# Kernel tuning notes

Measured on AMD Instinct MI355X. Metric: run time of the kernel, lower is better.

The kernel has to match this reference:

```python
import jax, jax.numpy as jnp
import numpy as np

L = 2        # rnn_layers
H = 512      # hidden size
T_MAX = 20   # text_max_len
V = 10000    # NUM_WORDS
B = 32       # batch
S = 49       # spatial positions (7x7)


def setup_inputs() -> dict:
    key = jax.random.key(0)
    ks = jax.random.split(key, 12)
    w = lambda k, shape: jax.random.normal(k, shape, dtype=jnp.float32) * 0.02
    return {
        "img_channels": jax.random.normal(ks[0], (B, 512, 7, 7), dtype=jnp.float32),
        "pooled": jax.random.normal(ks[1], (B, H), dtype=jnp.float32),
        "embed_table": w(ks[2], (V, H)),
        "Wq": w(ks[3], (H, H)), "bq": jnp.zeros((H,), jnp.float32),
        "Wk": w(ks[4], (S, S)), "bk": jnp.zeros((S,), jnp.float32),
        "Wv": w(ks[5], (S, S)), "bv": jnp.zeros((S,), jnp.float32),
        "Wih": w(ks[6], (L, 4 * H, H)), "Whh": w(ks[7], (L, 4 * H, H)),
        "bih": jnp.zeros((L, 4 * H), jnp.float32), "bhh": jnp.zeros((L, 4 * H), jnp.float32),
        "projW": w(ks[8], (V, H)), "projb": jnp.zeros((V,), jnp.float32),
        "hattW": w(ks[9], (H, 2 * H)), "hattb": jnp.zeros((H,), jnp.float32),
        "sos_idx": 1,
    }


def _lstm_cell(x, h, c, wih, whh, bi, bh):
    # PyTorch gate order: i, f, g, o
    g = x @ wih.T + bi + h @ whh.T + bh
    i, f, gg, o = jnp.split(g, 4, axis=-1)
    c2 = jax.nn.sigmoid(f) * c + jax.nn.sigmoid(i) * jnp.tanh(gg)
    return jax.nn.sigmoid(o) * jnp.tanh(c2), c2


def reference(img_channels, pooled, embed_table, Wq, bq, Wk, bk, Wv, bv,
              Wih, Whh, bih, bhh, projW, projb, hattW, hattb, sos_idx):
    Bsz = img_channels.shape[0]
    chan = img_channels.reshape(Bsz, 512, -1)           # [B,512,49]
    # keys/values are step-invariant: precompute once
    keys = jnp.tanh(chan @ Wk.T + bk)                    # [B,512,49]
    values = jnp.tanh(chan @ Wv.T + bv)                  # [B,512,49]

    emb0 = jnp.broadcast_to(embed_table[sos_idx], (Bsz, H))   # <SOS> embedding
    h0 = jnp.broadcast_to(pooled[None], (L, Bsz, H))
    c0 = h0

    def step(carry, _):
        emb, h, c = carry
        x = emb
        hs, cs = [], []
        for l in range(L):  # small fixed layer count
            hl, cl = _lstm_cell(x, h[l], c[l], Wih[l], Whh[l], bih[l], bhh[l])
            hs.append(hl); cs.append(cl)
            x = hl
        out = x                                          # [B,H] top-layer output
        h = jnp.stack(hs); c = jnp.stack(cs)
        # greedy next-token embedding (no teacher forcing)
        logits = out @ projW.T + projb                   # [B,V]
        emb_next = embed_table[jnp.argmax(logits, axis=-1)]
        # cross-attention gated hidden update (all layers at once)
        q = jnp.tanh(h @ Wq.T + bq)                      # [L,B,H]
        scores = jnp.einsum('lbd,bds->lbs', q, keys) / 7.0
        w = jax.nn.softmax(scores, axis=-1)              # [L,B,49]
        attn = jnp.einsum('lbs,bds->lbd', w, values)     # [L,B,H]
        h = jnp.tanh(jnp.concatenate([attn, h], axis=-1) @ hattW.T + hattb)
        return (emb_next, h, c), out

    _, outs = jax.lax.scan(step, (emb0, h0, c0), None, length=T_MAX - 1)
    pred = jnp.concatenate([emb0[None], outs], axis=0)   # [T,B,H]
    res = jnp.einsum('tbd,vd->bvt', pred, projW) + projb[None, :, None]
    return res                                           # [B,V,T]
```

## Files before the change

kernel.cpp:

```cpp
#include <hip/hip_runtime.h>

namespace {

constexpr int B = 32, H = 512, L = 2, T = 20, V = 10000, S = 49;

__device__ __forceinline__ float sigf(float x) { return 1.0f / (1.0f + expf(-x)); }
__device__ __forceinline__ float dot4(float4 a, float4 b) {
  return a.x*b.x + a.y*b.y + a.z*b.z + a.w*b.w;
}

__global__ __launch_bounds__(256) void setup_kernel(
    const float* __restrict__ chan,
    const float* __restrict__ Wk, const float* __restrict__ bk,
    const float* __restrict__ Wv, const float* __restrict__ bv,
    float* __restrict__ keysT, float* __restrict__ valuesT,
    const float* __restrict__ pooled, const float* __restrict__ embed,
    const int* __restrict__ sos,
    float* __restrict__ emb, float* __restrict__ h, float* __restrict__ c,
    const float* __restrict__ projW, const float* __restrict__ projb,
    float* __restrict__ slog0) {
  __shared__ __align__(16) float smem[8448];
  int blk = blockIdx.x, tid = threadIdx.x;
  if (blk < 256) {
    float* ch = smem;
    float* wk = smem + 64 * 52;
    float* wv = wk + 49 * 52;
    int b = blk >> 3, dt = blk & 7;
    for (int i = tid; i < 49 * 49; i += 256) {
      int s = i / 49, j = i % 49;
      wk[s * 52 + j] = Wk[i]; wv[s * 52 + j] = Wv[i];
    }
    for (int i = tid; i < 64 * 49; i += 256) {
      int d = i / 49, j = i % 49;
      ch[d * 52 + j] = chan[((size_t)b * 512 + dt * 64 + d) * S + j];
    }
    __syncthreads();
    int dl = tid >> 2, sq = tid & 3;
    for (int s = sq; s < S; s += 4) {
      float ak = bk[s], av = bv[s];
      for (int j = 0; j < 49; ++j) {
        float cv = ch[dl * 52 + j];
        ak += cv * wk[s * 52 + j];
        av += cv * wv[s * 52 + j];
      }
      int d = dt * 64 + dl;
      keysT[((size_t)b * S + s) * H + d] = tanhf(ak);
      valuesT[((size_t)b * S + s) * H + d] = tanhf(av);
    }
  } else if (blk < 384) {
    int idx = (blk - 256) * 256 + tid;
    float p = pooled[idx & (B * H - 1)];
    h[idx] = p;
    c[idx] = p;
    if (idx < B * H) emb[idx] = embed[(size_t)sos[0] * H + (idx & (H - 1))];
  } else {
    float* es = smem;
    es[tid] = embed[(size_t)sos[0] * H + tid];
    es[tid + 256] = embed[(size_t)sos[0] * H + tid + 256];
    __syncthreads();
    int ko = tid & 15, vl = tid >> 4;
    int v = (blk - 384) * 16 + vl;
    const float* wrow = projW + (size_t)v * H;
    float4 w[8];
#pragma unroll
    for (int kk = 0; kk < 8; ++kk) w[kk] = *(const float4*)&wrow[kk * 64 + ko * 4];
    float acc = 0.f;
#pragma unroll
    for (int kk = 0; kk < 8; ++kk)
      acc += dot4(*(const float4*)&es[kk * 64 + ko * 4], w[kk]);
    acc += __shfl_xor(acc, 1);
    acc += __shfl_xor(acc, 2);
    acc += __shfl_xor(acc, 4);
    acc += __shfl_xor(acc, 8);
    if (ko == 0) {
      float r = acc + projb[v];
      for (int b = 0; b < 32; ++b) slog0[(size_t)b * V + v] = r;
    }
  }
}

__global__ __launch_bounds__(256) void lstm_kernel(
    const float* __restrict__ x, const float* __restrict__ hprev,
    const float* __restrict__ cprev,
    const float* __restrict__ Wih, const float* __restrict__ Whh,
    const float* __restrict__ bih, const float* __restrict__ bhh,
    float* __restrict__ hout, float* __restrict__ cout) {
  __shared__ float gbuf[64];
  int tid = threadIdx.x;
  int hi = blockIdx.x >> 1, half = blockIdx.x & 1;
  int ko = tid & 15, rr = (tid >> 4) & 3, bh = tid >> 6;
  float acc[4];
#pragma unroll
  for (int j = 0; j < 4; ++j) acc[j] = 0.f;
  float4 w[8];
  {
    const float* wrow = Wih + ((size_t)rr * H + hi) * H;
#pragma unroll
    for (int kk = 0; kk < 8; ++kk) w[kk] = *(const float4*)&wrow[kk * 64 + ko * 4];
  }
#pragma unroll
  for (int j = 0; j < 4; ++j) {
    int b = half * 16 + bh * 4 + j;
    const float* xb = x + (size_t)b * H;
#pragma unroll
    for (int kk = 0; kk < 8; ++kk)
      acc[j] += dot4(*(const float4*)&xb[kk * 64 + ko * 4], w[kk]);
  }
  {
    const float* wrow = Whh + ((size_t)rr * H + hi) * H;
#pragma unroll
    for (int kk = 0; kk < 8; ++kk) w[kk] = *(const float4*)&wrow[kk * 64 + ko * 4];
  }
#pragma unroll
  for (int j = 0; j < 4; ++j) {
    int b = half * 16 + bh * 4 + j;
    const float* hb = hprev + (size_t)b * H;
#pragma unroll
    for (int kk = 0; kk < 8; ++kk)
      acc[j] += dot4(*(const float4*)&hb[kk * 64 + ko * 4], w[kk]);
  }
#pragma unroll
  for (int j = 0; j < 4; ++j) {
    acc[j] += __shfl_xor(acc[j], 1);
    acc[j] += __shfl_xor(acc[j], 2);
    acc[j] += __shfl_xor(acc[j], 4);
    acc[j] += __shfl_xor(acc[j], 8);
  }
  if (ko == 0) {
    float bias = bih[rr * H + hi] + bhh[rr * H + hi];
#pragma unroll
    for (int j = 0; j < 4; ++j) gbuf[rr * 16 + bh * 4 + j] = acc[j] + bias;
  }
  __syncthreads();
  if (tid < 16) {
    int b = half * 16 + tid;
    float gi = gbuf[tid], gf = gbuf[16 + tid], gg = gbuf[32 + tid], go = gbuf[48 + tid];
    float c2 = sigf(gf) * cprev[b * H + hi] + sigf(gi) * tanhf(gg);
    hout[b * H + hi] = sigf(go) * tanhf(c2);
    cout[b * H + hi] = c2;
  }
}

__global__ __launch_bounds__(256) void projsat_kernel(
    const float* __restrict__ hmid_all,
    const float* __restrict__ projW, const float* __restrict__ projb,
    const float* __restrict__ Wq, const float* __restrict__ bq,
    const float* __restrict__ keysT, const float* __restrict__ valuesT,
    float* __restrict__ dst, float* __restrict__ cat) {
  __shared__ __align__(16) float smem[1168];
  int blk = blockIdx.x, tid = threadIdx.x;
  if (blk < 1250) {
    const float* xin = hmid_all + B * H;
    int vchunk = blk >> 1, half = blk & 1;
    int ko = tid & 15, vl = tid >> 4;
    int v = vchunk * 16 + vl;
    const float* wrow = projW + (size_t)v * H;
    float4 w[8];
#pragma unroll
    for (int kk = 0; kk < 8; ++kk) w[kk] = *(const float4*)&wrow[kk * 64 + ko * 4];
    float acc[16];
#pragma unroll
    for (int bl = 0; bl < 16; ++bl) acc[bl] = 0.f;
#pragma unroll 4
    for (int bl = 0; bl < 16; ++bl) {
      const float* xb = xin + (size_t)(half * 16 + bl) * H;
#pragma unroll
      for (int kk = 0; kk < 8; ++kk)
        acc[bl] += dot4(*(const float4*)&xb[kk * 64 + ko * 4], w[kk]);
    }
#pragma unroll
    for (int bl = 0; bl < 16; ++bl) {
      acc[bl] += __shfl_xor(acc[bl], 1);
      acc[bl] += __shfl_xor(acc[bl], 2);
      acc[bl] += __shfl_xor(acc[bl], 4);
      acc[bl] += __shfl_xor(acc[bl], 8);
    }
    if (ko == 0) {
      float bias = projb[v];
      for (int bl = 0; bl < 16; ++bl)
        dst[(size_t)(half * 16 + bl) * V + v] = acc[bl] + bias;
    }
  } else {
    int lb = blk - 1250;
    int b = lb & 31, lg = lb >> 5;
    float* hr  = smem;
    float* qv  = smem + 512;
    float* scl = smem + 1040;
    float* wts = smem + 1104;
    const float* hrow = hmid_all + (size_t)lg * B * H + (size_t)b * H;
    hr[tid] = hrow[tid];
    hr[tid + 256] = hrow[tid + 256];
    __syncthreads();
    int ko = tid & 15, vl = tid >> 4;
    for (int jg = 0; jg < 32; ++jg) {
      int j = jg * 16 + vl;
      const float* wrow = Wq + (size_t)j * H;
      float4 w[8];
#pragma unroll
      for (int kk = 0; kk < 8; ++kk) w[kk] = *(const float4*)&wrow[kk * 64 + ko * 4];
      float acc = 0.f;
#pragma unroll
      for (int kk = 0; kk < 8; ++kk)
        acc += dot4(*(const float4*)&hr[kk * 64 + ko * 4], w[kk]);
      acc += __shfl_xor(acc, 1);
      acc += __shfl_xor(acc, 2);
      acc += __shfl_xor(acc, 4);
      acc += __shfl_xor(acc, 8);
      if (ko == 0) qv[(j >> 7) * 132 + (j & 127)] = tanhf(acc + bq[j]);
    }
    __syncthreads();
    int kq = tid & 3, sl = tid >> 2;
    float acc = 0.f;
    if (sl < S) {
      const float* kr = keysT + ((size_t)b * S + sl) * H + kq * 128;
      const float* qr = &qv[kq * 132];
      for (int k = 0; k < 128; k += 4)
        acc += dot4(*(const float4*)&qr[k], *(const float4*)&kr[k]);
    }
    acc += __shfl_xor(acc, 1);
    acc += __shfl_xor(acc, 2);
    if (kq == 0 && sl < S) scl[sl] = acc * (1.0f / 7.0f);
    __syncthreads();
    if (tid < 64) {
      float sc = (tid < S) ? scl[tid] : -3.4e38f;
      float m = sc;
      for (int o = 32; o > 0; o >>= 1) m = fmaxf(m, __shfl_xor(m, o));
      float e = (tid < S) ? expf(sc - m) : 0.f;
      float sum = e;
      for (int o = 32; o > 0; o >>= 1) sum += __shfl_xor(sum, o);
      if (tid < S) wts[tid] = e / sum;
    }
    __syncthreads();
    float acc0 = 0.f, acc1 = 0.f;
    for (int s = 0; s < S; ++s) {
      float w = wts[s];
      const float* vr = valuesT + ((size_t)b * S + s) * H;
      acc0 += w * vr[tid];
      acc1 += w * vr[tid + 256];
    }
    cat[lb * 1024 + tid] = acc0;
    cat[lb * 1024 + tid + 256] = acc1;
    cat[lb * 1024 + 512 + tid] = hmid_all[lb * H + tid];
    cat[lb * 1024 + 768 + tid] = hmid_all[lb * H + tid + 256];
  }
}

__global__ __launch_bounds__(256) void hattarg_kernel(
    const float* __restrict__ cat, const float* __restrict__ hattW,
    const float* __restrict__ hattb, float* __restrict__ h,
    const float* __restrict__ logits, const float* __restrict__ embed,
    float* __restrict__ emb) {
  __shared__ __align__(16) float smem[512];
  int blk = blockIdx.x, tid = threadIdx.x;
  if (blk < 256) {
    int lbg = blk & 7, jg = blk >> 3;
    int ko = tid & 15, jl = tid >> 4;
    int j = jg * 16 + jl;
    const float* wrow = hattW + (size_t)j * 1024;
    float4 w[16];
#pragma unroll
    for (int kk = 0; kk < 16; ++kk) w[kk] = *(const float4*)&wrow[kk * 64 + ko * 4];
    float acc[8];
#pragma unroll
    for (int ll = 0; ll < 8; ++ll) acc[ll] = 0.f;
#pragma unroll 2
    for (int ll = 0; ll < 8; ++ll) {
      const float* cb = cat + (size_t)(lbg * 8 + ll) * 1024;
#pragma unroll
      for (int kk = 0; kk < 16; ++kk)
        acc[ll] += dot4(*(const float4*)&cb[kk * 64 + ko * 4], w[kk]);
    }
#pragma unroll
    for (int ll = 0; ll < 8; ++ll) {
      acc[ll] += __shfl_xor(acc[ll], 1);
      acc[ll] += __shfl_xor(acc[ll], 2);
      acc[ll] += __shfl_xor(acc[ll], 4);
      acc[ll] += __shfl_xor(acc[ll], 8);
    }
    if (ko == 0) {
      float bias = hattb[j];
      for (int ll = 0; ll < 8; ++ll)
        h[(size_t)(lbg * 8 + ll) * H + j] = tanhf(acc[ll] + bias);
    }
  } else {
    int b = blk - 256;
    float* sv = smem;
    int* si = (int*)(smem + 256);
    float best = -3.4e38f;
    int bi = 0x7fffffff;
    for (int it = 0; it < 10; ++it) {
      int v0 = it * 1024 + tid * 4;
      if (v0 < V) {
        float4 lv = *(const float4*)&logits[(size_t)b * V + v0];
        if (lv.x > best) { best = lv.x; bi = v0; }
        if (lv.y > best) { best = lv.y; bi = v0 + 1; }
        if (lv.z > best) { best = lv.z; bi = v0 + 2; }
        if (lv.w > best) { best = lv.w; bi = v0 + 3; }
      }
    }
    sv[tid] = best; si[tid] = bi;
    __syncthreads();
    for (int st = 128; st > 0; st >>= 1) {
      if (tid < st) {
        float ov = sv[tid + st]; int oi = si[tid + st];
        if (ov > sv[tid] || (ov == sv[tid] && oi < si[tid])) { sv[tid] = ov; si[tid] = oi; }
      }
      __syncthreads();
    }
    int idx = si[0];
    for (int i = tid; i < H; i += 256) emb[b * H + i] = embed[(size_t)idx * H + i];
  }
}

__global__ __launch_bounds__(256) void finalize_kernel(
    const float* __restrict__ slog, float* __restrict__ outp) {
  int idx = blockIdx.x * 256 + threadIdx.x;
  float vals[T];
#pragma unroll
  for (int t = 0; t < T; ++t) vals[t] = slog[(size_t)t * (B * V) + idx];
#pragma unroll
  for (int t = 0; t < T; t += 4)
    *(float4*)&outp[(size_t)idx * T + t] =
        make_float4(vals[t], vals[t + 1], vals[t + 2], vals[t + 3]);
}


__global__ __launch_bounds__(256) void kv_kernel(
    const float* __restrict__ chan,
    const float* __restrict__ Wk, const float* __restrict__ bk,
    const float* __restrict__ Wv, const float* __restrict__ bv,
    float* __restrict__ keysT, float* __restrict__ valuesT) {
  __shared__ float ch[64][52];
  __shared__ float wk[49][52], wv[49][52];
  int b = blockIdx.x >> 3, dt = blockIdx.x & 7;
  int tid = threadIdx.x;
  for (int i = tid; i < 49 * 49; i += 256) {
    int s = i / 49, j = i % 49;
    wk[s][j] = Wk[i]; wv[s][j] = Wv[i];
  }
  for (int i = tid; i < 64 * 49; i += 256) {
    int d = i / 49, j = i % 49;
    ch[d][j] = chan[((size_t)b * 512 + dt * 64 + d) * S + j];
  }
  __syncthreads();
  int dl = tid >> 2, sq = tid & 3;
  for (int s = sq; s < S; s += 4) {
    float ak = bk[s], av = bv[s];
    for (int j = 0; j < 49; ++j) {
      float cv = ch[dl][j];
      ak += cv * wk[s][j];
      av += cv * wv[s][j];
    }
    int d = dt * 64 + dl;
    keysT[((size_t)b * S + s) * H + d] = tanhf(ak);
    valuesT[((size_t)b * S + s) * H + d] = tanhf(av);
  }
}

__global__ void init_kernel(const float* __restrict__ pooled,
                            const float* __restrict__ embed,
                            const int* __restrict__ sos,
                            float* __restrict__ emb, float* __restrict__ h,
                            float* __restrict__ c) {
  int idx = blockIdx.x * 256 + threadIdx.x;
  float p = pooled[idx & (B * H - 1)];
  h[idx] = p;
  c[idx] = p;
  if (idx < B * H) emb[idx] = embed[sos[0] * H + (idx & (H - 1))];
}

__global__ __launch_bounds__(256) void lstm_kernel_fb(
    const float* __restrict__ x, const float* __restrict__ hprev,
    const float* __restrict__ cprev,
    const float* __restrict__ Wih, const float* __restrict__ Whh,
    const float* __restrict__ bih, const float* __restrict__ bhh,
    float* __restrict__ hout, float* __restrict__ cout) {
  __shared__ __align__(16) float smem[32 * 512];
  int tid = threadIdx.x;
  int hi = blockIdx.x;
  int ko = tid & 15, rr = (tid >> 4) & 3, bh = tid >> 6;
  {
    const float4* xg = (const float4*)x;
    float4* s4 = (float4*)smem;
    for (int i = tid; i < 4096; i += 256) s4[i] = xg[i];
  }
  __syncthreads();
  float acc[8];
#pragma unroll
  for (int j = 0; j < 8; ++j) acc[j] = 0.f;
  {
    const float* wrow = Wih + ((size_t)rr * H + hi) * H;
    float4 w[8];
#pragma unroll
    for (int kk = 0; kk < 8; ++kk) w[kk] = *(const float4*)&wrow[kk * 64 + ko * 4];
#pragma unroll
    for (int j = 0; j < 8; ++j) {
      const float* xb = smem + (bh * 8 + j) * 512;
#pragma unroll
      for (int kk = 0; kk < 8; ++kk)
        acc[j] += dot4(*(const float4*)&xb[kk * 64 + ko * 4], w[kk]);
    }
  }
  __syncthreads();
  {
    const float4* hg = (const float4*)hprev;
    float4* s4 = (float4*)smem;
    for (int i = tid; i < 4096; i += 256) s4[i] = hg[i];
  }
  __syncthreads();
  {
    const float* wrow = Whh + ((size_t)rr * H + hi) * H;
    float4 w[8];
#pragma unroll
    for (int kk = 0; kk < 8; ++kk) w[kk] = *(const float4*)&wrow[kk * 64 + ko * 4];
#pragma unroll
    for (int j = 0; j < 8; ++j) {
      const float* xb = smem + (bh * 8 + j) * 512;
#pragma unroll
      for (int kk = 0; kk < 8; ++kk)
        acc[j] += dot4(*(const float4*)&xb[kk * 64 + ko * 4], w[kk]);
    }
  }
  __syncthreads();
#pragma unroll
  for (int j = 0; j < 8; ++j) {
    acc[j] += __shfl_xor(acc[j], 1);
    acc[j] += __shfl_xor(acc[j], 2);
    acc[j] += __shfl_xor(acc[j], 4);
    acc[j] += __shfl_xor(acc[j], 8);
  }
  float* gbuf = smem;
  if (ko == 0) {
    float bias = bih[rr * H + hi] + bhh[rr * H + hi];
#pragma unroll
    for (int j = 0; j < 8; ++j) gbuf[rr * 32 + bh * 8 + j] = acc[j] + bias;
  }
  __syncthreads();
  if (tid < 32) {
    int b = tid;
    float gi = gbuf[b], gf = gbuf[32 + b], gg = gbuf[64 + b], go = gbuf[96 + b];
    float c2 = sigf(gf) * cprev[b * H + hi] + sigf(gi) * tanhf(gg);
    hout[b * H + hi] = sigf(go) * tanhf(c2);
    cout[b * H + hi] = c2;
  }
}

__global__ __launch_bounds__(256) void projq_kernel(
    const float* __restrict__ xin,
    const float* __restrict__ projW, const float* __restrict__ projb,
    float* __restrict__ logits, float* __restrict__ ocol, int direct, int tcol,
    const float* __restrict__ hmid_all, const float* __restrict__ Wq,
    const float* __restrict__ bq, float* __restrict__ q) {
  __shared__ __align__(16) float xs[32 * 512];
  int blk = blockIdx.x, tid = threadIdx.x;
  int ko = tid & 15, vl = tid >> 4;
  if (blk < 625) {
    {
      const float4* xg = (const float4*)xin;
      float4* s4 = (float4*)xs;
      for (int i = tid; i < 4096; i += 256) s4[i] = xg[i];
    }
    __syncthreads();
    int v = blk * 16 + vl;
    const float* wrow = projW + (size_t)v * H;
    float4 w[8];
#pragma unroll
    for (int kk = 0; kk < 8; ++kk) w[kk] = *(const float4*)&wrow[kk * 64 + ko * 4];
    float acc[32];
#pragma unroll
    for (int b = 0; b < 32; ++b) acc[b] = 0.f;
    for (int b = 0; b < 32; ++b) {
      const float* xb = xs + b * 512;
#pragma unroll
      for (int kk = 0; kk < 8; ++kk)
        acc[b] += dot4(*(const float4*)&xb[kk * 64 + ko * 4], w[kk]);
    }
#pragma unroll
    for (int b = 0; b < 32; ++b) {
      acc[b] += __shfl_xor(acc[b], 1);
      acc[b] += __shfl_xor(acc[b], 2);
      acc[b] += __shfl_xor(acc[b], 4);
      acc[b] += __shfl_xor(acc[b], 8);
    }
    if (ko == 0) {
      float bias = projb[v];
      for (int b = 0; b < 32; ++b) {
        float r = acc[b] + bias;
        logits[b * V + v] = r;
        if (direct) ocol[((size_t)b * V + v) * T + tcol] = r;
        else        ocol[b * V + v] = r;
      }
    }
  } else {
    int b2 = blk - 625;
    int lg = b2 & 1, jg = b2 >> 1;
    {
      const float4* xg = (const float4*)(hmid_all + lg * 32 * H);
      float4* s4 = (float4*)xs;
      for (int i = tid; i < 4096; i += 256) s4[i] = xg[i];
    }
    __syncthreads();
    int j = jg * 16 + vl;
    const float* wrow = Wq + (size_t)j * H;
    float4 w[8];
#pragma unroll
    for (int kk = 0; kk < 8; ++kk) w[kk] = *(const float4*)&wrow[kk * 64 + ko * 4];
    float acc[32];
#pragma unroll
    for (int b = 0; b < 32; ++b) acc[b] = 0.f;
    for (int b = 0; b < 32; ++b) {
      const float* xb = xs + b * 512;
#pragma unroll
      for (int kk = 0; kk < 8; ++kk)
        acc[b] += dot4(*(const float4*)&xb[kk * 64 + ko * 4], w[kk]);
    }
#pragma unroll
    for (int b = 0; b < 32; ++b) {
      acc[b] += __shfl_xor(acc[b], 1);
      acc[b] += __shfl_xor(acc[b], 2);
      acc[b] += __shfl_xor(acc[b], 4);
      acc[b] += __shfl_xor(acc[b], 8);
    }
    if (ko == 0) {
      float bias = bq[j];
      for (int b = 0; b < 32; ++b)
        q[(lg * 32 + b) * H + j] = tanhf(acc[b] + bias);
    }
  }
}

__global__ __launch_bounds__(256) void sattn_kernel(
    const float* __restrict__ q, const float* __restrict__ keysT,
    const float* __restrict__ valuesT, const float* __restrict__ hmid,
    float* __restrict__ cat) {
  __shared__ __align__(16) float qv[528];
  __shared__ float scl[64];
  __shared__ float wts[64];
  int lb = blockIdx.x, tid = threadIdx.x;
  int b = lb & 31;
  {
    int c0 = tid, c1 = tid + 256;
    qv[(c0 >> 7) * 132 + (c0 & 127)] = q[lb * H + c0];
    qv[(c1 >> 7) * 132 + (c1 & 127)] = q[lb * H + c1];
  }
  __syncthreads();
  int kq = tid & 3, sl = tid >> 2;
  float acc = 0.f;
  if (sl < S) {
    const float* kr = keysT + ((size_t)b * S + sl) * H + kq * 128;
    const float* qr = &qv[kq * 132];
    for (int k = 0; k < 128; k += 4)
      acc += dot4(*(const float4*)&qr[k], *(const float4*)&kr[k]);
  }
  acc += __shfl_xor(acc, 1);
  acc += __shfl_xor(acc, 2);
  if (kq == 0 && sl < S) scl[sl] = acc * (1.0f / 7.0f);
  __syncthreads();
  if (tid < 64) {
    float sc = (tid < S) ? scl[tid] : -3.4e38f;
    float m = sc;
    for (int o = 32; o > 0; o >>= 1) m = fmaxf(m, __shfl_xor(m, o));
    float e = (tid < S) ? expf(sc - m) : 0.f;
    float sum = e;
    for (int o = 32; o > 0; o >>= 1) sum += __shfl_xor(sum, o);
    if (tid < S) wts[tid] = e / sum;
  }
  __syncthreads();
  float acc0 = 0.f, acc1 = 0.f;
  for (int s = 0; s < S; ++s) {
    float w = wts[s];
    const float* vr = valuesT + ((size_t)b * S + s) * H;
    acc0 += w * vr[tid];
    acc1 += w * vr[tid + 256];
  }
  cat[lb * 1024 + tid] = acc0;
  cat[lb * 1024 + tid + 256] = acc1;
  cat[lb * 1024 + 512 + tid] = hmid[lb * H + tid];
  cat[lb * 1024 + 768 + tid] = hmid[lb * H + tid + 256];
}

__global__ __launch_bounds__(256) void hattarg_kernel_fb(
    const float* __restrict__ cat, const float* __restrict__ hattW,
    const float* __restrict__ hattb, float* __restrict__ h,
    const float* __restrict__ logits, const float* __restrict__ embed,
    float* __restrict__ emb) {
  __shared__ __align__(16) float smem[16 * 1024];
  int blk = blockIdx.x, tid = threadIdx.x;
  if (blk < 128) {
    int lbg = blk & 3, jg = blk >> 2;
    {
      const float4* cg2 = (const float4*)(cat + lbg * 16 * 1024);
      float4* s4 = (float4*)smem;
      for (int i = tid; i < 4096; i += 256) s4[i] = cg2[i];
    }
    __syncthreads();
    int ko = tid & 15, jl = tid >> 4;
    int j = jg * 16 + jl;
    const float* wrow = hattW + (size_t)j * 1024;
    float4 w[16];
#pragma unroll
    for (int kk = 0; kk < 16; ++kk) w[kk] = *(const float4*)&wrow[kk * 64 + ko * 4];
    float acc[16];
#pragma unroll
    for (int lb = 0; lb < 16; ++lb) acc[lb] = 0.f;
    for (int lb = 0; lb < 16; ++lb) {
      const float* cb = smem + lb * 1024;
#pragma unroll
      for (int kk = 0; kk < 16; ++kk)
        acc[lb] += dot4(*(const float4*)&cb[kk * 64 + ko * 4], w[kk]);
    }
#pragma unroll
    for (int lb = 0; lb < 16; ++lb) {
      acc[lb] += __shfl_xor(acc[lb], 1);
      acc[lb] += __shfl_xor(acc[lb], 2);
      acc[lb] += __shfl_xor(acc[lb], 4);
      acc[lb] += __shfl_xor(acc[lb], 8);
    }
    if (ko == 0) {
      float bias = hattb[j];
      for (int lb = 0; lb < 16; ++lb)
        h[(lbg * 16 + lb) * H + j] = tanhf(acc[lb] + bias);
    }
  } else {
    int b = blk - 128;
    float* sv = smem;
    int* si = (int*)(smem + 256);
    float best = -3.4e38f;
    int bi = 0x7fffffff;
    for (int it = 0; it < 10; ++it) {
      int v0 = it * 1024 + tid * 4;
      if (v0 < V) {
        float4 lv = *(const float4*)&logits[b * V + v0];
        if (lv.x > best) { best = lv.x; bi = v0; }
        if (lv.y > best) { best = lv.y; bi = v0 + 1; }
        if (lv.z > best) { best = lv.z; bi = v0 + 2; }
        if (lv.w > best) { best = lv.w; bi = v0 + 3; }
      }
    }
    sv[tid] = best; si[tid] = bi;
    __syncthreads();
    for (int st = 128; st > 0; st >>= 1) {
      if (tid < st) {
        float ov = sv[tid + st]; int oi = si[tid + st];
        if (ov > sv[tid] || (ov == sv[tid] && oi < si[tid])) { sv[tid] = ov; si[tid] = oi; }
      }
      __syncthreads();
    }
    int idx = si[0];
    for (int i = tid; i < H; i += 256) emb[b * H + i] = embed[(size_t)idx * H + i];
  }
}

}

extern "C" void kernel_launch(void* const* d_in, const int* in_sizes, int n_in,
                              void* d_out, int out_size, void* d_ws, size_t ws_size,
                              hipStream_t stream) {
  (void)in_sizes; (void)n_in; (void)out_size;
  const float* chan   = (const float*)d_in[0];
  const float* pooled = (const float*)d_in[1];
  const float* embed  = (const float*)d_in[2];
  const float* Wq     = (const float*)d_in[3];
  const float* bq     = (const float*)d_in[4];
  const float* Wk     = (const float*)d_in[5];
  const float* bk     = (const float*)d_in[6];
  const float* Wv     = (const float*)d_in[7];
  const float* bv     = (const float*)d_in[8];
  const float* Wih    = (const float*)d_in[9];
  const float* Whh    = (const float*)d_in[10];
  const float* bih    = (const float*)d_in[11];
  const float* bhh    = (const float*)d_in[12];
  const float* projW  = (const float*)d_in[13];
  const float* projb  = (const float*)d_in[14];
  const float* hattW  = (const float*)d_in[15];
  const float* hattb  = (const float*)d_in[16];
  const int*   sos    = (const int*)d_in[17];

  float* out = (float*)d_out;
  float* ws  = (float*)d_ws;

  float* keysT   = ws;
  float* valuesT = keysT + B * S * 512;
  float* emb     = valuesT + B * S * 512;
  float* h       = emb + B * H;
  float* c       = h + L * B * H;
  float* hmid    = c + L * B * H;
  float* cat     = hmid + L * B * H;
  float* q       = cat + L * B * 1024;
  float* logits  = q + L * B * H;
  float* slog    = logits + B * V;

  size_t base_floats = (size_t)(slog - ws);
  bool staged = ws_size >= (base_floats + (size_t)T * B * V) * sizeof(float);

  if (staged) {
    setup_kernel<<<1009, 256, 0, stream>>>(chan, Wk, bk, Wv, bv, keysT, valuesT,
                                           pooled, embed, sos, emb, h, c,
                                           projW, projb, slog);
    for (int t = 0; t < T - 1; ++t) {
      float* dst = slog + (size_t)(t + 1) * B * V;
      lstm_kernel<<<1024, 256, 0, stream>>>(emb, h, c, Wih, Whh, bih, bhh, hmid, c);
      lstm_kernel<<<1024, 256, 0, stream>>>(hmid, h + B * H, c + B * H,
                                            Wih + 4 * H * H, Whh + 4 * H * H,
                                            bih + 4 * H, bhh + 4 * H,
                                            hmid + B * H, c + B * H);
      bool last = (t == T - 2);
      projsat_kernel<<<last ? 1250 : 1314, 256, 0, stream>>>(
          hmid, projW, projb, Wq, bq, keysT, valuesT, dst, cat);
      if (!last)
        hattarg_kernel<<<288, 256, 0, stream>>>(cat, hattW, hattb, h,
                                                dst, embed, emb);
    }
    finalize_kernel<<<(B * V) / 256, 256, 0, stream>>>(slog, out);
    return;
  }

  kv_kernel<<<256, 256, 0, stream>>>(chan, Wk, bk, Wv, bv, keysT, valuesT);
  init_kernel<<<(L * B * H) / 256, 256, 0, stream>>>(pooled, embed, sos, emb, h, c);
  projq_kernel<<<625, 256, 0, stream>>>(emb, projW, projb, logits, out,
                                        1, 0, hmid, Wq, bq, q);
  for (int t = 0; t < T - 1; ++t) {
    lstm_kernel_fb<<<512, 256, 0, stream>>>(emb, h, c, Wih, Whh, bih, bhh, hmid, c);
    lstm_kernel_fb<<<512, 256, 0, stream>>>(hmid, h + B * H, c + B * H,
                                            Wih + 4 * H * H, Whh + 4 * H * H,
                                            bih + 4 * H, bhh + 4 * H,
                                            hmid + B * H, c + B * H);
    projq_kernel<<<689, 256, 0, stream>>>(hmid + B * H, projW, projb, logits, out,
                                          1, t + 1, hmid, Wq, bq, q);
    sattn_kernel<<<L * B, 256, 0, stream>>>(q, keysT, valuesT, hmid, cat);
    hattarg_kernel_fb<<<160, 256, 0, stream>>>(cat, hattW, hattb, h,
                                               logits, embed, emb);
  }
}
```

Measured before the change: 2.229 ms.

## Stage activations in double-buffered LDS and widen per-block batch coverage in GEMV kernels

The LSTM, projection and hidden-attention kernels now cover all 32 batch rows (or 16 for hatt) per block instead of splitting the batch across two blocks. Activations are staged through a double-buffered shared-memory tile, loaded into registers one chunk ahead. This halves the grid sizes so each weight row is read from global memory once per step, and replaces repeated global activation reads with LDS reads. In exchange, blocks use far more shared memory and more accumulator registers, which may reduce occupancy, and the fewer, larger blocks may leave CUs idle.

```diff
diff --git a/kernel.cpp b/kernel.cpp
--- a/kernel.cpp
+++ b/kernel.cpp
@@ -85,56 +85,73 @@
     const float* __restrict__ Wih, const float* __restrict__ Whh,
     const float* __restrict__ bih, const float* __restrict__ bhh,
     float* __restrict__ hout, float* __restrict__ cout) {
-  __shared__ float gbuf[64];
+  __shared__ __align__(16) float smem[8192];
   int tid = threadIdx.x;
-  int hi = blockIdx.x >> 1, half = blockIdx.x & 1;
+  int hi = blockIdx.x;
   int ko = tid & 15, rr = (tid >> 4) & 3, bh = tid >> 6;
-  float acc[4];
-#pragma unroll
-  for (int j = 0; j < 4; ++j) acc[j] = 0.f;
-  float4 w[8];
+  float4 w1[8], w2[8];
   {
     const float* wrow = Wih + ((size_t)rr * H + hi) * H;
 #pragma unroll
-    for (int kk = 0; kk < 8; ++kk) w[kk] = *(const float4*)&wrow[kk * 64 + ko * 4];
-  }
-#pragma unroll
-  for (int j = 0; j < 4; ++j) {
-    int b = half * 16 + bh * 4 + j;
-    const float* xb = x + (size_t)b * H;
-#pragma unroll
-    for (int kk = 0; kk < 8; ++kk)
-      acc[j] += dot4(*(const float4*)&xb[kk * 64 + ko * 4], w[kk]);
+    for (int kk = 0; kk < 8; ++kk) w1[kk] = *(const float4*)&wrow[kk * 64 + ko * 4];
   }
   {
     const float* wrow = Whh + ((size_t)rr * H + hi) * H;
 #pragma unroll
-    for (int kk = 0; kk < 8; ++kk) w[kk] = *(const float4*)&wrow[kk * 64 + ko * 4];
-  }
-#pragma unroll
-  for (int j = 0; j < 4; ++j) {
-    int b = half * 16 + bh * 4 + j;
-    const float* hb = hprev + (size_t)b * H;
-#pragma unroll
-    for (int kk = 0; kk < 8; ++kk)
-      acc[j] += dot4(*(const float4*)&hb[kk * 64 + ko * 4], w[kk]);
-  }
-#pragma unroll
-  for (int j = 0; j < 4; ++j) {
+    for (int kk = 0; kk < 8; ++kk) w2[kk] = *(const float4*)&wrow[kk * 64 + ko * 4];
+  }
+  float acc[8];
+#pragma unroll
+  for (int j = 0; j < 8; ++j) acc[j] = 0.f;
+
+  float4 st[4];
+#pragma unroll
+  for (int it = 0; it < 4; ++it) {
+    int i = it * 256 + tid;
+    st[it] = *(const float4*)&x[(i >> 5) * H + (i & 31) * 4];
+  }
+#pragma unroll 1
+  for (int kt = 0; kt < 8; ++kt) {
+    float4* buf4 = (float4*)(smem + (kt & 1) * 4096);
+#pragma unroll
+    for (int it = 0; it < 4; ++it) buf4[it * 256 + tid] = st[it];
+    __syncthreads();
+    if (kt < 7) {
+      const float* src = (kt < 3) ? x : hprev;
+      int kt2 = (kt + 1) & 3;
+#pragma unroll
+      for (int it = 0; it < 4; ++it) {
+        int i = it * 256 + tid;
+        st[it] = *(const float4*)&src[(i >> 5) * H + kt2 * 128 + (i & 31) * 4];
+      }
+    }
+    const float* bs = smem + (kt & 1) * 4096;
+    const float4* w = (kt < 4) ? w1 : w2;
+    int k0 = (kt & 3) * 2;
+#pragma unroll
+    for (int j = 0; j < 8; ++j) {
+      const float* xb = bs + (bh * 8 + j) * 128;
+      acc[j] += dot4(*(const float4*)&xb[ko * 4], w[k0]);
+      acc[j] += dot4(*(const float4*)&xb[64 + ko * 4], w[k0 + 1]);
+    }
+  }
+#pragma unroll
+  for (int j = 0; j < 8; ++j) {
     acc[j] += __shfl_xor(acc[j], 1);
     acc[j] += __shfl_xor(acc[j], 2);
     acc[j] += __shfl_xor(acc[j], 4);
     acc[j] += __shfl_xor(acc[j], 8);
   }
+  float* gbuf = smem;
   if (ko == 0) {
     float bias = bih[rr * H + hi] + bhh[rr * H + hi];
 #pragma unroll
-    for (int j = 0; j < 4; ++j) gbuf[rr * 16 + bh * 4 + j] = acc[j] + bias;
-  }
-  __syncthreads();
-  if (tid < 16) {
-    int b = half * 16 + tid;
-    float gi = gbuf[tid], gf = gbuf[16 + tid], gg = gbuf[32 + tid], go = gbuf[48 + tid];
+    for (int j = 0; j < 8; ++j) gbuf[rr * 32 + bh * 8 + j] = acc[j] + bias;
+  }
+  __syncthreads();
+  if (tid < 32) {
+    int b = tid;
+    float gi = gbuf[b], gf = gbuf[32 + b], gg = gbuf[64 + b], go = gbuf[96 + b];
     float c2 = sigf(gf) * cprev[b * H + hi] + sigf(gi) * tanhf(gg);
     hout[b * H + hi] = sigf(go) * tanhf(c2);
     cout[b * H + hi] = c2;
@@ -147,41 +164,60 @@
     const float* __restrict__ Wq, const float* __restrict__ bq,
     const float* __restrict__ keysT, const float* __restrict__ valuesT,
     float* __restrict__ dst, float* __restrict__ cat) {
-  __shared__ __align__(16) float smem[1168];
+  __shared__ __align__(16) float smem[8192];
   int blk = blockIdx.x, tid = threadIdx.x;
-  if (blk < 1250) {
+  if (blk < 625) {
     const float* xin = hmid_all + B * H;
-    int vchunk = blk >> 1, half = blk & 1;
     int ko = tid & 15, vl = tid >> 4;
-    int v = vchunk * 16 + vl;
+    int v = blk * 16 + vl;
     const float* wrow = projW + (size_t)v * H;
     float4 w[8];
 #pragma unroll
     for (int kk = 0; kk < 8; ++kk) w[kk] = *(const float4*)&wrow[kk * 64 + ko * 4];
-    float acc[16];
-#pragma unroll
-    for (int bl = 0; bl < 16; ++bl) acc[bl] = 0.f;
-#pragma unroll 4
-    for (int bl = 0; bl < 16; ++bl) {
-      const float* xb = xin + (size_t)(half * 16 + bl) * H;
-#pragma unroll
-      for (int kk = 0; kk < 8; ++kk)
-        acc[bl] += dot4(*(const float4*)&xb[kk * 64 + ko * 4], w[kk]);
-    }
-#pragma unroll
-    for (int bl = 0; bl < 16; ++bl) {
-      acc[bl] += __shfl_xor(acc[bl], 1);
-      acc[bl] += __shfl_xor(acc[bl], 2);
-      acc[bl] += __shfl_xor(acc[bl], 4);
-      acc[bl] += __shfl_xor(acc[bl], 8);
+    float acc[32];
+#pragma unroll
+    for (int b = 0; b < 32; ++b) acc[b] = 0.f;
+    float4 st[4];
+#pragma unroll
+    for (int it = 0; it < 4; ++it) {
+      int i = it * 256 + tid;
+      st[it] = *(const float4*)&xin[(i >> 5) * H + (i & 31) * 4];
+    }
+#pragma unroll 1
+    for (int kt = 0; kt < 4; ++kt) {
+      float4* buf4 = (float4*)(smem + (kt & 1) * 4096);
+#pragma unroll
+      for (int it = 0; it < 4; ++it) buf4[it * 256 + tid] = st[it];
+      __syncthreads();
+      if (kt < 3) {
+#pragma unroll
+        for (int it = 0; it < 4; ++it) {
+          int i = it * 256 + tid;
+          st[it] = *(const float4*)&xin[(i >> 5) * H + (kt + 1) * 128 + (i & 31) * 4];
+        }
+      }
+      const float* bs = smem + (kt & 1) * 4096;
+      int k0 = kt * 2;
+#pragma unroll
+      for (int b = 0; b < 32; ++b) {
+        const float* xb = bs + b * 128;
+        acc[b] += dot4(*(const float4*)&xb[ko * 4], w[k0]);
+        acc[b] += dot4(*(const float4*)&xb[64 + ko * 4], w[k0 + 1]);
+      }
+    }
+#pragma unroll
+    for (int b = 0; b < 32; ++b) {
+      acc[b] += __shfl_xor(acc[b], 1);
+      acc[b] += __shfl_xor(acc[b], 2);
+      acc[b] += __shfl_xor(acc[b], 4);
+      acc[b] += __shfl_xor(acc[b], 8);
     }
     if (ko == 0) {
       float bias = projb[v];
-      for (int bl = 0; bl < 16; ++bl)
-        dst[(size_t)(half * 16 + bl) * V + v] = acc[bl] + bias;
+      for (int b = 0; b < 32; ++b) dst[(size_t)b * V + v] = acc[b] + bias;
     }
   } else {
-    int lb = blk - 1250;
+    int lb = blk - 625;
     int b = lb & 31, lg = lb >> 5;
     float* hr  = smem;
     float* qv  = smem + 512;
@@ -250,40 +286,63 @@
     const float* __restrict__ hattb, float* __restrict__ h,
     const float* __restrict__ logits, const float* __restrict__ embed,
     float* __restrict__ emb) {
-  __shared__ __align__(16) float smem[512];
+  __shared__ __align__(16) float smem[8192];
   int blk = blockIdx.x, tid = threadIdx.x;
-  if (blk < 256) {
-    int lbg = blk & 7, jg = blk >> 3;
+  if (blk < 128) {
+    int lbg = blk & 3, jg = blk >> 2;
     int ko = tid & 15, jl = tid >> 4;
     int j = jg * 16 + jl;
     const float* wrow = hattW + (size_t)j * 1024;
     float4 w[16];
 #pragma unroll
     for (int kk = 0; kk < 16; ++kk) w[kk] = *(const float4*)&wrow[kk * 64 + ko * 4];
-    float acc[8];
-#pragma unroll
-    for (int ll = 0; ll < 8; ++ll) acc[ll] = 0.f;
-#pragma unroll 2
-    for (int ll = 0; ll < 8; ++ll) {
-      const float* cb = cat + (size_t)(lbg * 8 + ll) * 1024;
-#pragma unroll
-      for (int kk = 0; kk < 16; ++kk)
-        acc[ll] += dot4(*(const float4*)&cb[kk * 64 + ko * 4], w[kk]);
-    }
-#pragma unroll
-    for (int ll = 0; ll < 8; ++ll) {
-      acc[ll] += __shfl_xor(acc[ll], 1);
-      acc[ll] += __shfl_xor(acc[ll], 2);
-      acc[ll] += __shfl_xor(acc[ll], 4);
-      acc[ll] += __shfl_xor(acc[ll], 8);
+    float acc[16];
+#pragma unroll
+    for (int lb = 0; lb < 16; ++lb) acc[lb] = 0.f;
+    const float* csrc = cat + (size_t)lbg * 16 * 1024;
+    float4 st[4];
+#pragma unroll
+    for (int it = 0; it < 4; ++it) {
+      int i = it * 256 + tid;
+      st[it] = *(const float4*)&csrc[(i >> 6) * 1024 + (i & 63) * 4];
+    }
+#pragma unroll 1
+    for (int kt = 0; kt < 4; ++kt) {
+      float4* buf4 = (float4*)(smem + (kt & 1) * 4096);
+#pragma unroll
+      for (int it = 0; it < 4; ++it) buf4[it * 256 + tid] = st[it];
+      __syncthreads();
+      if (kt < 3) {
+#pragma unroll
+        for (int it = 0; it < 4; ++it) {
+          int i = it * 256 + tid;
+          st[it] = *(const float4*)&csrc[(i >> 6) * 1024 + (kt + 1) * 256 + (i & 63) * 4];
+        }
+      }
+      const float* bs = smem + (kt & 1) * 4096;
+      int k0 = kt * 4;
+#pragma unroll
+      for (int lb = 0; lb < 16; ++lb) {
+        const float* cb = bs + lb * 256;
+#pragma unroll
+        for (int kx = 0; kx < 4; ++kx)
+          acc[lb] += dot4(*(const float4*)&cb[kx * 64 + ko * 4], w[k0 + kx]);
+      }
+    }
+#pragma unroll
+    for (int lb = 0; lb < 16; ++lb) {
+      acc[lb] += __shfl_xor(acc[lb], 1);
+      acc[lb] += __shfl_xor(acc[lb], 2);
+      acc[lb] += __shfl_xor(acc[lb], 4);
+      acc[lb] += __shfl_xor(acc[lb], 8);
     }
     if (ko == 0) {
       float bias = hattb[j];
-      for (int ll = 0; ll < 8; ++ll)
-        h[(size_t)(lbg * 8 + ll) * H + j] = tanhf(acc[ll] + bias);
+      for (int lb = 0; lb < 16; ++lb)
+        h[(size_t)(lbg * 16 + lb) * H + j] = tanhf(acc[lb] + bias);
     }
   } else {
-    int b = blk - 256;
+    int b = blk - 128;
     float* sv = smem;
     int* si = (int*)(smem + 256);
     float best = -3.4e38f;
@@ -699,16 +758,16 @@
                                            projW, projb, slog);
     for (int t = 0; t < T - 1; ++t) {
       float* dst = slog + (size_t)(t + 1) * B * V;
-      lstm_kernel<<<1024, 256, 0, stream>>>(emb, h, c, Wih, Whh, bih, bhh, hmid, c);
-      lstm_kernel<<<1024, 256, 0, stream>>>(hmid, h + B * H, c + B * H,
-                                            Wih + 4 * H * H, Whh + 4 * H * H,
-                                            bih + 4 * H, bhh + 4 * H,
-                                            hmid + B * H, c + B * H);
+      lstm_kernel<<<512, 256, 0, stream>>>(emb, h, c, Wih, Whh, bih, bhh, hmid, c);
+      lstm_kernel<<<512, 256, 0, stream>>>(hmid, h + B * H, c + B * H,
+                                           Wih + 4 * H * H, Whh + 4 * H * H,
+                                           bih + 4 * H, bhh + 4 * H,
+                                           hmid + B * H, c + B * H);
       bool last = (t == T - 2);
-      projsat_kernel<<<last ? 1250 : 1314, 256, 0, stream>>>(
+      projsat_kernel<<<last ? 625 : 689, 256, 0, stream>>>(
           hmid, projW, projb, Wq, bq, keysT, valuesT, dst, cat);
       if (!last)
-        hattarg_kernel<<<288, 256, 0, stream>>>(cat, hattW, hattb, h,
+        hattarg_kernel<<<160, 256, 0, stream>>>(cat, hattW, hattb, h,
                                                 dst, embed, emb);
     }
     finalize_kernel<<<(B * V) / 256, 256, 0, stream>>>(slog, out);
```

After: 2.532 ms. +13.6%, slower.
